# Optimization experiments

Measured on AMD Instinct MI355X. Metric: run time of the kernel, lower is better.

Reference implementation:

```python
import jax, jax.numpy as jnp
import numpy as np

BATCH = 65536
IN_FEATURES = 128
OUT_FEATURES = 128
GRID = 8  # initial_grid: number of RBF/spline basis centers per edge


def setup_inputs() -> dict:
    key = jax.random.key(0)
    k1, k2, k3 = jax.random.split(key, 3)
    x = jax.random.normal(k1, (BATCH, IN_FEATURES), dtype=jnp.float32)
    # Per-edge spline coefficients stacked: [out, in, grid]
    coeffs = jax.random.normal(k2, (OUT_FEATURES, IN_FEATURES, GRID), dtype=jnp.float32) * 0.1
    # Per-edge base (SiLU) weights stacked: [out, in]
    base_w = jax.random.normal(k3, (OUT_FEATURES, IN_FEATURES), dtype=jnp.float32) * 0.1
    # Shared uniform grid of RBF centers in [-1, 1]
    centers = jnp.linspace(-1.0, 1.0, GRID, dtype=jnp.float32)
    return {"x": x, "coeffs": coeffs, "base_w": base_w, "centers": centers}


def reference(x, coeffs, base_w, centers):
    # HybridBasisFunction per edge: base_w * silu(x) + sum_g coeffs[g] * exp(-((x-c_g)/w)^2)
    width = 2.0 / (GRID - 1)  # grid spacing
    # basis: [B, in, G]
    diff = (x[:, :, None] - centers[None, None, :]) / width
    basis = jnp.exp(-diff * diff)
    # Sum over all edges (j -> i): output[b, i] = sum_j phi_ij(x[b, j])
    out = jnp.einsum('big,oig->bo', basis, coeffs)
    out = out + jnp.einsum('bi,oi->bo', jax.nn.silu(x), base_w)
    return out
```

## Files before the change

### kernel.cpp

```cpp
#include <hip/hip_runtime.h>

typedef __fp16       pk16x2 __attribute__((ext_vector_type(2)));
typedef _Float16     f16x8  __attribute__((ext_vector_type(8)));
typedef float        f32x4  __attribute__((ext_vector_type(4)));
typedef float        f32x16 __attribute__((ext_vector_type(16)));
typedef unsigned int u32x4  __attribute__((ext_vector_type(4)));

#define BATCH 65536
#define NIN   128
#define NOUT  128

#define L2E   1.4426950408889634f
#define SQL2E 1.2011224087864498f
#define EM2   0.1353352832366127f


__global__ __launch_bounds__(256) void kan_prep(const float* __restrict__ coeffs,
                                                const float* __restrict__ base_w,
                                                _Float16* __restrict__ W3) {
    int t = blockIdx.x * 256 + threadIdx.x;
    int ks   = t >> 8;
    int c    = t & 255;
    int nbb  = c >> 6;
    int lane = c & 63;
    int sub  = lane >> 5;
    int col  = nbb * 32 + (lane & 31);
    f16x8 v;
    if (ks < 64) {
        int g = ks >> 3, t2 = ks & 7;
        const float* src = coeffs + ((size_t)col * 128 + g * 16 + sub * 8 + t2) * 8;
#pragma unroll
        for (int e = 0; e < 8; ++e) v[e] = (_Float16)src[e];
    } else {
        const float* src = base_w + (size_t)col * 128 + (ks - 64) * 16 + sub * 8;
#pragma unroll
        for (int e = 0; e < 8; ++e) v[e] = (_Float16)src[e];
    }
    *(f16x8*)((char*)W3 + (size_t)t * 16) = v;
}

__device__ __forceinline__ void gll16(const void* g, void* l) {
    __builtin_amdgcn_global_load_lds(
        (const __attribute__((address_space(1))) unsigned int*)g,
        (__attribute__((address_space(3))) unsigned int*)l, 16, 0, 0);
}

__device__ __forceinline__ f16x8 basis8r(float t) {
    float u  = t * SQL2E;
    float b0 = __builtin_amdgcn_exp2f(-(u * u));
    float r  = __builtin_amdgcn_exp2f(__builtin_fmaf(t, 2.0f * L2E, -L2E));
    float b1 = b0 * r; r *= EM2;
    float b2 = b1 * r; r *= EM2;
    float b3 = b2 * r; r *= EM2;
    float b4 = b3 * r; r *= EM2;
    float b5 = b4 * r; r *= EM2;
    float b6 = b5 * r; r *= EM2;
    float b7 = b6 * r;
    u32x4 U;
    U[0] = __builtin_bit_cast(unsigned int, __builtin_amdgcn_cvt_pkrtz(b0, b1));
    U[1] = __builtin_bit_cast(unsigned int, __builtin_amdgcn_cvt_pkrtz(b2, b3));
    U[2] = __builtin_bit_cast(unsigned int, __builtin_amdgcn_cvt_pkrtz(b4, b5));
    U[3] = __builtin_bit_cast(unsigned int, __builtin_amdgcn_cvt_pkrtz(b6, b7));
    return __builtin_bit_cast(f16x8, U);
}

__device__ __forceinline__ float silu1(float xv) {
    float p = __builtin_amdgcn_exp2f(-xv * L2E);
    return xv * __builtin_amdgcn_rcpf(1.0f + p);
}

__global__ __launch_bounds__(256, 2) void kan_main(const float* __restrict__ x,
                                                   const _Float16* __restrict__ W3,
                                                   float* __restrict__ out) {
    __shared__ _Float16 smem[2][16384];

    const int tid  = threadIdx.x;
    const int lane = tid & 63;
    const int w    = tid >> 6;
    const int l31  = lane & 31;
    const int sub  = lane >> 5;
    const int row0 = blockIdx.x * 128 + w * 32;

    const float* xp = x + (size_t)(row0 + l31) * NIN;

    f32x16 accA[4], accB[4];
#pragma unroll
    for (int q = 0; q < 4; ++q)
#pragma unroll
        for (int r = 0; r < 16; ++r) { accA[q][r] = 0.f; accB[q][r] = 0.f; }

    const char* wbase = (const char*)W3;
#define STAGE(buf, grp)                                                         \
    do {                                                                        \
        const char* _s = wbase + (size_t)(grp) * 32768 + (size_t)tid * 16;      \
        char*       _d = (char*)&smem[(buf)][0] + (size_t)tid * 16;             \
        _Pragma("unroll")                                                       \
        for (int _i = 0; _i < 8; ++_i) gll16(_s + _i * 4096, _d + _i * 4096);   \
    } while (0)

    STAGE(0, 0);
    f32x4 xa = *(const f32x4*)(xp + sub * 8);
    f32x4 xb = *(const f32x4*)(xp + sub * 8 + 4);
    __syncthreads();

#pragma unroll
    for (int g = 0; g < 8; ++g) {
        const int cur = g & 1;
        STAGE(cur ^ 1, g + 1);
        const int nxt = (g < 7) ? (g + 1) * 16 : 0;
        f32x4 xa2 = *(const f32x4*)(xp + nxt + sub * 8);
        f32x4 xb2 = *(const f32x4*)(xp + nxt + sub * 8 + 4);

        f16x8 a[8];
#pragma unroll
        for (int t2 = 0; t2 < 4; ++t2) a[t2]     = basis8r(__builtin_fmaf(xa[t2], 3.5f, 3.5f));
#pragma unroll
        for (int t2 = 0; t2 < 4; ++t2) a[4 + t2] = basis8r(__builtin_fmaf(xb[t2], 3.5f, 3.5f));

#pragma unroll
        for (int tp = 0; tp < 4; ++tp) {
            const char* bpa = (const char*)&smem[cur][0] + (tp * 2) * 4096 + lane * 16;
            const char* bpb = bpa + 4096;
#pragma unroll
            for (int q = 0; q < 4; ++q) {
                f16x8 b = *(const f16x8*)(bpa + q * 1024);
                accA[q] = __builtin_amdgcn_mfma_f32_32x32x16_f16(a[tp * 2], b, accA[q], 0, 0, 0);
            }
#pragma unroll
            for (int q = 0; q < 4; ++q) {
                f16x8 b = *(const f16x8*)(bpb + q * 1024);
                accB[q] = __builtin_amdgcn_mfma_f32_32x32x16_f16(a[tp * 2 + 1], b, accB[q], 0, 0, 0);
            }
        }
        xa = xa2; xb = xb2;
        __syncthreads();
    }

#pragma unroll
    for (int sp = 0; sp < 4; ++sp) {
#pragma unroll
        for (int half = 0; half < 2; ++half) {
            const int s = sp * 2 + half;
            f32x4 xa2, xb2;
            if (s < 7) {
                xa2 = *(const f32x4*)(xp + (s + 1) * 16 + sub * 8);
                xb2 = *(const f32x4*)(xp + (s + 1) * 16 + sub * 8 + 4);
            }
            u32x4 U;
            U[0] = __builtin_bit_cast(unsigned int,
                   __builtin_amdgcn_cvt_pkrtz(silu1(xa[0]), silu1(xa[1])));
            U[1] = __builtin_bit_cast(unsigned int,
                   __builtin_amdgcn_cvt_pkrtz(silu1(xa[2]), silu1(xa[3])));
            U[2] = __builtin_bit_cast(unsigned int,
                   __builtin_amdgcn_cvt_pkrtz(silu1(xb[0]), silu1(xb[1])));
            U[3] = __builtin_bit_cast(unsigned int,
                   __builtin_amdgcn_cvt_pkrtz(silu1(xb[2]), silu1(xb[3])));
            f16x8 a = __builtin_bit_cast(f16x8, U);
            const char* bp = (const char*)&smem[0][0] + s * 4096 + lane * 16;
            if (half == 0) {
#pragma unroll
                for (int q = 0; q < 4; ++q) {
                    f16x8 bq = *(const f16x8*)(bp + q * 1024);
                    accA[q] = __builtin_amdgcn_mfma_f32_32x32x16_f16(a, bq, accA[q], 0, 0, 0);
                }
            } else {
#pragma unroll
                for (int q = 0; q < 4; ++q) {
                    f16x8 bq = *(const f16x8*)(bp + q * 1024);
                    accB[q] = __builtin_amdgcn_mfma_f32_32x32x16_f16(a, bq, accB[q], 0, 0, 0);
                }
            }
            if (s < 7) { xa = xa2; xb = xb2; }
        }
    }

#pragma unroll
    for (int q = 0; q < 4; ++q)
#pragma unroll
        for (int r = 0; r < 16; ++r) {
            int crow = (r & 3) + 8 * (r >> 2) + 4 * sub;
            out[(size_t)(row0 + crow) * NOUT + q * 32 + l31] = accA[q][r] + accB[q][r];
        }
}

extern "C" void kernel_launch(void* const* d_in, const int* in_sizes, int n_in,
                              void* d_out, int out_size, void* d_ws, size_t ws_size,
                              hipStream_t stream) {
    const float* x       = (const float*)d_in[0];
    const float* coeffs  = (const float*)d_in[1];
    const float* base_w  = (const float*)d_in[2];
    _Float16* W3 = (_Float16*)d_ws;

    kan_prep<<<dim3(72), dim3(256), 0, stream>>>(coeffs, base_w, W3);
    kan_main<<<dim3(BATCH / 128), dim3(256), 0, stream>>>(x, W3, (float*)d_out);
}
```

Measured before the change: 38.34 us.

## Drop LDS weight staging and retile waves to 64x64 with direct global weight loads

Removes the double-buffered LDS staging of the packed fp16 weights and the per-group barriers. Each wave now reads its B fragments straight from global memory, relying on the L1/L2 caches. The work split changes so each wave covers 64 rows by 64 output columns, and paired blocks split the columns. This removes barrier and LDS traffic, but each row's Gaussian basis and SiLU values are now computed twice (once per column half), x is loaded twice, and weight loads now carry global-memory latency.

```diff
diff --git a/kernel.cpp b/kernel.cpp
--- a/kernel.cpp
+++ b/kernel.cpp
@@ -1,6 +1,5 @@
 #include <hip/hip_runtime.h>
 
-typedef __fp16       pk16x2 __attribute__((ext_vector_type(2)));
 typedef _Float16     f16x8  __attribute__((ext_vector_type(8)));
 typedef float        f32x4  __attribute__((ext_vector_type(4)));
 typedef float        f32x16 __attribute__((ext_vector_type(16)));
@@ -39,12 +38,6 @@
     *(f16x8*)((char*)W3 + (size_t)t * 16) = v;
 }
 
-__device__ __forceinline__ void gll16(const void* g, void* l) {
-    __builtin_amdgcn_global_load_lds(
-        (const __attribute__((address_space(1))) unsigned int*)g,
-        (__attribute__((address_space(3))) unsigned int*)l, 16, 0, 0);
-}
-
 __device__ __forceinline__ f16x8 basis8r(float t) {
     float u  = t * SQL2E;
     float b0 = __builtin_amdgcn_exp2f(-(u * u));
@@ -72,115 +65,109 @@
 __global__ __launch_bounds__(256, 2) void kan_main(const float* __restrict__ x,
                                                    const _Float16* __restrict__ W3,
                                                    float* __restrict__ out) {
-    __shared__ _Float16 smem[2][16384];
-
     const int tid  = threadIdx.x;
     const int lane = tid & 63;
     const int w    = tid >> 6;
     const int l31  = lane & 31;
     const int sub  = lane >> 5;
-    const int row0 = blockIdx.x * 128 + w * 32;
+    const int h    = blockIdx.x & 1;
+    const int row0 = (blockIdx.x >> 1) * 256 + w * 64;
+    const int col0 = h * 64;
 
     const float* xp = x + (size_t)(row0 + l31) * NIN;
+    const char*  wb = (const char*)W3 + col0 * 32 + lane * 16;
 
-    f32x16 accA[4], accB[4];
+    f32x16 acc[2][2];
 #pragma unroll
-    for (int q = 0; q < 4; ++q)
+    for (int m = 0; m < 2; ++m)
 #pragma unroll
-        for (int r = 0; r < 16; ++r) { accA[q][r] = 0.f; accB[q][r] = 0.f; }
+        for (int q = 0; q < 2; ++q)
+#pragma unroll
+            for (int r = 0; r < 16; ++r) acc[m][q][r] = 0.f;
 
-    const char* wbase = (const char*)W3;
-#define STAGE(buf, grp)                                                         \
-    do {                                                                        \
-        const char* _s = wbase + (size_t)(grp) * 32768 + (size_t)tid * 16;      \
-        char*       _d = (char*)&smem[(buf)][0] + (size_t)tid * 16;             \
-        _Pragma("unroll")                                                       \
-        for (int _i = 0; _i < 8; ++_i) gll16(_s + _i * 4096, _d + _i * 4096);   \
-    } while (0)
-
-    STAGE(0, 0);
-    f32x4 xa = *(const f32x4*)(xp + sub * 8);
-    f32x4 xb = *(const f32x4*)(xp + sub * 8 + 4);
-    __syncthreads();
+    f32x4 xa0 = *(const f32x4*)(xp + sub * 8);
+    f32x4 xa1 = *(const f32x4*)(xp + sub * 8 + 4);
+    f32x4 xb0 = *(const f32x4*)(xp + 16 * 256 + sub * 8);
+    f32x4 xb1 = *(const f32x4*)(xp + 16 * 256 + sub * 8 + 4);
 
 #pragma unroll
     for (int g = 0; g < 8; ++g) {
-        const int cur = g & 1;
-        STAGE(cur ^ 1, g + 1);
         const int nxt = (g < 7) ? (g + 1) * 16 : 0;
-        f32x4 xa2 = *(const f32x4*)(xp + nxt + sub * 8);
-        f32x4 xb2 = *(const f32x4*)(xp + nxt + sub * 8 + 4);
+        f32x4 na0 = *(const f32x4*)(xp + nxt + sub * 8);
+        f32x4 na1 = *(const f32x4*)(xp + nxt + sub * 8 + 4);
+        f32x4 nb0 = *(const f32x4*)(xp + 4096 + nxt + sub * 8);
+        f32x4 nb1 = *(const f32x4*)(xp + 4096 + nxt + sub * 8 + 4);
 
-        f16x8 a[8];
+        f16x8 aA[8], aB[8];
 #pragma unroll
-        for (int t2 = 0; t2 < 4; ++t2) a[t2]     = basis8r(__builtin_fmaf(xa[t2], 3.5f, 3.5f));
-#pragma unroll
-        for (int t2 = 0; t2 < 4; ++t2) a[4 + t2] = basis8r(__builtin_fmaf(xb[t2], 3.5f, 3.5f));
+        for (int t2 = 0; t2 < 4; ++t2) {
+            aA[t2]     = basis8r(__builtin_fmaf(xa0[t2], 3.5f, 3.5f));
+            aA[4 + t2] = basis8r(__builtin_fmaf(xa1[t2], 3.5f, 3.5f));
+            aB[t2]     = basis8r(__builtin_fmaf(xb0[t2], 3.5f, 3.5f));
+            aB[4 + t2] = basis8r(__builtin_fmaf(xb1[t2], 3.5f, 3.5f));
+        }
 
 #pragma unroll
-        for (int tp = 0; tp < 4; ++tp) {
-            const char* bpa = (const char*)&smem[cur][0] + (tp * 2) * 4096 + lane * 16;
-            const char* bpb = bpa + 4096;
-#pragma unroll
-            for (int q = 0; q < 4; ++q) {
-                f16x8 b = *(const f16x8*)(bpa + q * 1024);
-                accA[q] = __builtin_amdgcn_mfma_f32_32x32x16_f16(a[tp * 2], b, accA[q], 0, 0, 0);
-            }
-#pragma unroll
-            for (int q = 0; q < 4; ++q) {
-                f16x8 b = *(const f16x8*)(bpb + q * 1024);
-                accB[q] = __builtin_amdgcn_mfma_f32_32x32x16_f16(a[tp * 2 + 1], b, accB[q], 0, 0, 0);
-            }
+        for (int t2 = 0; t2 < 8; ++t2) {
+            const char* bp = wb + (size_t)(g * 8 + t2) * 4096;
+            f16x8 b0 = *(const f16x8*)bp;
+            f16x8 b1 = *(const f16x8*)(bp + 1024);
+            acc[0][0] = __builtin_amdgcn_mfma_f32_32x32x16_f16(aA[t2], b0, acc[0][0], 0, 0, 0);
+            acc[0][1] = __builtin_amdgcn_mfma_f32_32x32x16_f16(aA[t2], b1, acc[0][1], 0, 0, 0);
+            acc[1][0] = __builtin_amdgcn_mfma_f32_32x32x16_f16(aB[t2], b0, acc[1][0], 0, 0, 0);
+            acc[1][1] = __builtin_amdgcn_mfma_f32_32x32x16_f16(aB[t2], b1, acc[1][1], 0, 0, 0);
         }
-        xa = xa2; xb = xb2;
-        __syncthreads();
+        xa0 = na0; xa1 = na1; xb0 = nb0; xb1 = nb1;
     }
 
 #pragma unroll
-    for (int sp = 0; sp < 4; ++sp) {
-#pragma unroll
-        for (int half = 0; half < 2; ++half) {
-            const int s = sp * 2 + half;
-            f32x4 xa2, xb2;
-            if (s < 7) {
-                xa2 = *(const f32x4*)(xp + (s + 1) * 16 + sub * 8);
-                xb2 = *(const f32x4*)(xp + (s + 1) * 16 + sub * 8 + 4);
-            }
-            u32x4 U;
-            U[0] = __builtin_bit_cast(unsigned int,
-                   __builtin_amdgcn_cvt_pkrtz(silu1(xa[0]), silu1(xa[1])));
-            U[1] = __builtin_bit_cast(unsigned int,
-                   __builtin_amdgcn_cvt_pkrtz(silu1(xa[2]), silu1(xa[3])));
-            U[2] = __builtin_bit_cast(unsigned int,
-                   __builtin_amdgcn_cvt_pkrtz(silu1(xb[0]), silu1(xb[1])));
-            U[3] = __builtin_bit_cast(unsigned int,
-                   __builtin_amdgcn_cvt_pkrtz(silu1(xb[2]), silu1(xb[3])));
-            f16x8 a = __builtin_bit_cast(f16x8, U);
-            const char* bp = (const char*)&smem[0][0] + s * 4096 + lane * 16;
-            if (half == 0) {
-#pragma unroll
-                for (int q = 0; q < 4; ++q) {
-                    f16x8 bq = *(const f16x8*)(bp + q * 1024);
-                    accA[q] = __builtin_amdgcn_mfma_f32_32x32x16_f16(a, bq, accA[q], 0, 0, 0);
-                }
-            } else {
-#pragma unroll
-                for (int q = 0; q < 4; ++q) {
-                    f16x8 bq = *(const f16x8*)(bp + q * 1024);
-                    accB[q] = __builtin_amdgcn_mfma_f32_32x32x16_f16(a, bq, accB[q], 0, 0, 0);
-                }
-            }
-            if (s < 7) { xa = xa2; xb = xb2; }
+    for (int s = 0; s < 8; ++s) {
+        f32x4 na0, na1, nb0, nb1;
+        if (s < 7) {
+            na0 = *(const f32x4*)(xp + (s + 1) * 16 + sub * 8);
+            na1 = *(const f32x4*)(xp + (s + 1) * 16 + sub * 8 + 4);
+            nb0 = *(const f32x4*)(xp + 4096 + (s + 1) * 16 + sub * 8);
+            nb1 = *(const f32x4*)(xp + 4096 + (s + 1) * 16 + sub * 8 + 4);
         }
+        u32x4 UA, UB;
+        UA[0] = __builtin_bit_cast(unsigned int,
+                __builtin_amdgcn_cvt_pkrtz(silu1(xa0[0]), silu1(xa0[1])));
+        UA[1] = __builtin_bit_cast(unsigned int,
+                __builtin_amdgcn_cvt_pkrtz(silu1(xa0[2]), silu1(xa0[3])));
+        UA[2] = __builtin_bit_cast(unsigned int,
+                __builtin_amdgcn_cvt_pkrtz(silu1(xa1[0]), silu1(xa1[1])));
+        UA[3] = __builtin_bit_cast(unsigned int,
+                __builtin_amdgcn_cvt_pkrtz(silu1(xa1[2]), silu1(xa1[3])));
+        UB[0] = __builtin_bit_cast(unsigned int,
+                __builtin_amdgcn_cvt_pkrtz(silu1(xb0[0]), silu1(xb0[1])));
+        UB[1] = __builtin_bit_cast(unsigned int,
+                __builtin_amdgcn_cvt_pkrtz(silu1(xb0[2]), silu1(xb0[3])));
+        UB[2] = __builtin_bit_cast(unsigned int,
+                __builtin_amdgcn_cvt_pkrtz(silu1(xb1[0]), silu1(xb1[1])));
+        UB[3] = __builtin_bit_cast(unsigned int,
+                __builtin_amdgcn_cvt_pkrtz(silu1(xb1[2]), silu1(xb1[3])));
+        f16x8 aA = __builtin_bit_cast(f16x8, UA);
+        f16x8 aB = __builtin_bit_cast(f16x8, UB);
+        const char* bp = wb + (size_t)(64 + s) * 4096;
+        f16x8 b0 = *(const f16x8*)bp;
+        f16x8 b1 = *(const f16x8*)(bp + 1024);
+        acc[0][0] = __builtin_amdgcn_mfma_f32_32x32x16_f16(aA, b0, acc[0][0], 0, 0, 0);
+        acc[0][1] = __builtin_amdgcn_mfma_f32_32x32x16_f16(aA, b1, acc[0][1], 0, 0, 0);
+        acc[1][0] = __builtin_amdgcn_mfma_f32_32x32x16_f16(aB, b0, acc[1][0], 0, 0, 0);
+        acc[1][1] = __builtin_amdgcn_mfma_f32_32x32x16_f16(aB, b1, acc[1][1], 0, 0, 0);
+        if (s < 7) { xa0 = na0; xa1 = na1; xb0 = nb0; xb1 = nb1; }
     }
 
 #pragma unroll
-    for (int q = 0; q < 4; ++q)
+    for (int m = 0; m < 2; ++m)
 #pragma unroll
-        for (int r = 0; r < 16; ++r) {
-            int crow = (r & 3) + 8 * (r >> 2) + 4 * sub;
-            out[(size_t)(row0 + crow) * NOUT + q * 32 + l31] = accA[q][r] + accB[q][r];
-        }
+        for (int q = 0; q < 2; ++q)
+#pragma unroll
+            for (int r = 0; r < 16; ++r) {
+                int crow = (r & 3) + 8 * (r >> 2) + 4 * sub;
+                out[(size_t)(row0 + m * 32 + crow) * NOUT + col0 + q * 32 + l31] =
+                    acc[m][q][r];
+            }
 }
 
 extern "C" void kernel_launch(void* const* d_in, const int* in_sizes, int n_in,
```

New measurement: 46.43 us. 21.1% more time.
